# Optimization experiments

Measured on AMD Instinct MI355X. Metric: run time of the kernel, lower is better.

## Reference

```python
import jax, jax.numpy as jnp
import numpy as np
from jax import lax

WINDOW_SIZE = 11
PAD = WINDOW_SIZE // 2
L = 128.0
C1 = (0.01 * L) ** 2  # 1.6384
C2 = (0.03 * L) ** 2  # 14.7456


def _box(x, window):
    # depthwise (grouped) conv with uniform 11x11 box window, SAME padding
    return lax.conv_general_dilated(
        x, window, window_strides=(1, 1), padding=[(PAD, PAD), (PAD, PAD)],
        dimension_numbers=("NCHW", "OIHW", "NCHW"),
        feature_group_count=x.shape[1])


def setup_inputs() -> dict:
    key = jax.random.key(0)
    k1, k2 = jax.random.split(key)
    B, Ch, H, W = 64, 1, 512, 512
    img1 = jax.random.normal(k1, (B, Ch, H, W), dtype=jnp.float32)
    img2 = jax.random.normal(k2, (B, Ch, H, W), dtype=jnp.float32)
    # uniform normalized box window: outer(ones/11, ones/11) -> 1/121 each
    window = jnp.full((Ch, 1, WINDOW_SIZE, WINDOW_SIZE), 1.0 / (WINDOW_SIZE ** 2),
                      dtype=jnp.float32)
    return {"img1": img1, "img2": img2, "window": window}


def reference(img1, img2, window):
    mu1 = _box(img1, window)
    mu2 = _box(img2, window)
    mu1_sq = mu1 * mu1
    mu2_sq = mu2 * mu2
    mu1_mu2 = mu1 * mu2
    sigma1_sq = _box(img1 * img1, window) - mu1_sq
    sigma2_sq = _box(img2 * img2, window) - mu2_sq
    sigma12 = _box(img1 * img2, window) - mu1_mu2
    ret = (2.0 * mu1_mu2 + C1) / (mu1_sq + mu2_sq + C1)
    cs = (2.0 * sigma12 + C2) / (sigma1_sq + sigma2_sq + C2)
    ssim_map = ret * cs  # non_neg_flag=False, mask=None
    return 1.0 - jnp.mean(ssim_map)  # size_average=True
```

## Files before the change

kernel.cpp:

```cpp
#include <hip/hip_runtime.h>
#include <hip/hip_bf16.h>

namespace {

constexpr int IMG_H = 512;
constexpr int IMG_W = 512;
constexpr int BATCH = 64;
constexpr int RT = 16;
constexpr int WAVES = 4;
constexpr int ROWS_PER_BLOCK = RT * WAVES;
constexpr int BLOCKS_PER_IMG = IMG_H / ROWS_PER_BLOCK;
constexpr int GRID = BATCH * BLOCKS_PER_IMG;
constexpr int NPART = GRID * WAVES;
constexpr float C1 = 1.6384f;
constexpr float C2 = 14.7456f;
constexpr float INV121 = 1.0f / 121.0f;

__device__ __forceinline__ float shup1(float v) { return __shfl_up(v, 1, 64); }
__device__ __forceinline__ float shdn1(float v) { return __shfl_down(v, 1, 64); }

template <bool ADD>
__device__ __forceinline__ void hrow_acc(const float* __restrict__ p1,
                                         const float* __restrict__ p2,
                                         int r, int lane, int c0,
                                         float V[5][8])
{
  if ((unsigned)r >= (unsigned)IMG_H) return;
  const float4* a1 = reinterpret_cast<const float4*>(p1 + (size_t)r * IMG_W + c0);
  const float4* a2 = reinterpret_cast<const float4*>(p2 + (size_t)r * IMG_W + c0);
  float4 xa = a1[0], xb = a1[1];
  float4 ya = a2[0], yb = a2[1];
  float ox[8] = {xa.x, xa.y, xa.z, xa.w, xb.x, xb.y, xb.z, xb.w};
  float oy[8] = {ya.x, ya.y, ya.z, ya.w, yb.x, yb.y, yb.z, yb.w};

  float xw[18], yw[18];
#pragma unroll
  for (int i = 0; i < 8; ++i) { xw[5 + i] = ox[i]; yw[5 + i] = oy[i]; }
  const bool l0 = (lane == 0), l63 = (lane == 63);
#pragma unroll
  for (int i = 0; i < 5; ++i) {
    float tx = shup1(ox[3 + i]), ty = shup1(oy[3 + i]);
    xw[i] = l0 ? 0.f : tx;
    yw[i] = l0 ? 0.f : ty;
    float bx = shdn1(ox[i]), by = shdn1(oy[i]);
    xw[13 + i] = l63 ? 0.f : bx;
    yw[13 + i] = l63 ? 0.f : by;
  }

#pragma unroll
  for (int q = 0; q < 5; ++q) {
    float w[18];
#pragma unroll
    for (int j = 0; j < 18; ++j) {
      float xv = xw[j], yv = yw[j];
      w[j] = (q == 0) ? xv
           : (q == 1) ? yv
           : (q == 2) ? xv * xv
           : (q == 3) ? yv * yv
           : xv * yv;
    }
    float h = w[0];
#pragma unroll
    for (int j = 1; j < 11; ++j) h += w[j];
    V[q][0] += ADD ? h : -h;
#pragma unroll
    for (int k = 1; k < 8; ++k) {
      h += w[k + 10] - w[k - 1];
      V[q][k] += ADD ? h : -h;
    }
  }
}

__device__ __forceinline__ float ssim_row(const float V[5][8])
{
  float rs = 0.f;
#pragma unroll
  for (int k = 0; k < 8; ++k) {
    float mu1 = V[0][k] * INV121;
    float mu2 = V[1][k] * INV121;
    float m11 = mu1 * mu1, m22 = mu2 * mu2, m12 = mu1 * mu2;
    float s1  = V[2][k] * INV121 - m11;
    float s2  = V[3][k] * INV121 - m22;
    float s12 = V[4][k] * INV121 - m12;
    float n1 = 2.f * m12 + C1;
    float n2 = 2.f * s12 + C2;
    float d1 = m11 + m22 + C1;
    float d2 = s1 + s2 + C2;
    float den = d1 * d2;
    float rc = __builtin_amdgcn_rcpf(den);
    rc = rc * (2.f - den * rc);
    rs += (n1 * n2) * rc;
  }
  return rs;
}

}

__global__ __launch_bounds__(256, 2) void ssim_main(
    const float* __restrict__ img1, const float* __restrict__ img2,
    float* __restrict__ partials)
{
  const int tid = threadIdx.x;
  const int wave = tid >> 6;
  const int lane = tid & 63;
  const int gb = blockIdx.x;
  const int b  = gb >> 3;
  const int rb = gb & 7;
  const int y0 = rb * ROWS_PER_BLOCK + wave * RT;
  const int c0 = lane * 8;
  const float* p1 = img1 + (size_t)b * IMG_H * IMG_W;
  const float* p2 = img2 + (size_t)b * IMG_H * IMG_W;

  float V[5][8];
#pragma unroll
  for (int q = 0; q < 5; ++q)
#pragma unroll
    for (int k = 0; k < 8; ++k) V[q][k] = 0.f;

#pragma unroll 1
  for (int d = -5; d <= 5; ++d) hrow_acc<true>(p1, p2, y0 + d, lane, c0, V);

  float acc = ssim_row(V);

#pragma unroll 1
  for (int y = y0 + 1; y < y0 + RT; ++y) {
    hrow_acc<true >(p1, p2, y + 5, lane, c0, V);
    hrow_acc<false>(p1, p2, y - 6, lane, c0, V);
    acc += ssim_row(V);
  }

#pragma unroll
  for (int off = 32; off > 0; off >>= 1) acc += __shfl_down(acc, off, 64);
  if (lane == 0) partials[gb * WAVES + wave] = acc;
}

__global__ void ssim_reduce(const float* __restrict__ partials,
                            float* __restrict__ out)
{
  __shared__ double sd[256];
  const int tid = threadIdx.x;
  double s = 0.0;
  for (int i = tid; i < NPART; i += 256) s += (double)partials[i];
  sd[tid] = s;
  __syncthreads();
  for (int st = 128; st > 0; st >>= 1) {
    if (tid < st) sd[tid] += sd[tid + st];
    __syncthreads();
  }
  if (tid == 0) {
    double mean = sd[0] * (1.0 / 16777216.0);
    out[0] = (float)(1.0 - mean);
  }
}

extern "C" void kernel_launch(void* const* d_in, const int* in_sizes, int n_in,
                              void* d_out, int out_size, void* d_ws, size_t ws_size,
                              hipStream_t stream)
{
  const float* img1 = (const float*)d_in[0];
  const float* img2 = (const float*)d_in[1];
  float* out = (float*)d_out;
  float* partials = (float*)d_ws;

  ssim_main<<<dim3(GRID), dim3(256), 0, stream>>>(img1, img2, partials);
  ssim_reduce<<<dim3(1), dim3(256), 0, stream>>>(partials, out);
}
```

Measured before the change: 184.5 us.

## Swap separable box filter order: vertical running sums then horizontal pass

The kernel now keeps vertical running column sums of the five moment quantities per pixel, updated by adding the entering row and subtracting the leaving row. The horizontal 11-tap sliding sum is computed once per output row on these column sums. Before, it ran on every input row twice, once to add and once to subtract. This roughly halves the shuffle and horizontal-add work per output row. It also halves rows per wave, which doubles the grid and the halo reloads, and raises the occupancy hint to 4 blocks per CU, which may pressure registers.

```diff
diff --git a/kernel.cpp b/kernel.cpp
--- a/kernel.cpp
+++ b/kernel.cpp
@@ -6,7 +6,7 @@
 constexpr int IMG_H = 512;
 constexpr int IMG_W = 512;
 constexpr int BATCH = 64;
-constexpr int RT = 16;
+constexpr int RT = 8;
 constexpr int WAVES = 4;
 constexpr int ROWS_PER_BLOCK = RT * WAVES;
 constexpr int BLOCKS_PER_IMG = IMG_H / ROWS_PER_BLOCK;
@@ -20,10 +20,9 @@
 __device__ __forceinline__ float shdn1(float v) { return __shfl_down(v, 1, 64); }
 
 template <bool ADD>
-__device__ __forceinline__ void hrow_acc(const float* __restrict__ p1,
+__device__ __forceinline__ void vrow_acc(const float* __restrict__ p1,
                                          const float* __restrict__ p2,
-                                         int r, int lane, int c0,
-                                         float V[5][8])
+                                         int r, int c0, float V[5][8])
 {
   if ((unsigned)r >= (unsigned)IMG_H) return;
   const float4* a1 = reinterpret_cast<const float4*>(p1 + (size_t)r * IMG_W + c0);
@@ -32,56 +31,55 @@
   float4 ya = a2[0], yb = a2[1];
   float ox[8] = {xa.x, xa.y, xa.z, xa.w, xb.x, xb.y, xb.z, xb.w};
   float oy[8] = {ya.x, ya.y, ya.z, ya.w, yb.x, yb.y, yb.z, yb.w};
+#pragma unroll
+  for (int k = 0; k < 8; ++k) {
+    float x = ox[k], y = oy[k];
+    if (ADD) {
+      V[0][k] += x;       V[1][k] += y;
+      V[2][k] += x * x;   V[3][k] += y * y;   V[4][k] += x * y;
+    } else {
+      V[0][k] -= x;       V[1][k] -= y;
+      V[2][k] -= x * x;   V[3][k] -= y * y;   V[4][k] -= x * y;
+    }
+  }
+}
 
-  float xw[18], yw[18];
-#pragma unroll
-  for (int i = 0; i < 8; ++i) { xw[5 + i] = ox[i]; yw[5 + i] = oy[i]; }
+__device__ __forceinline__ float ssim_from_V(const float V[5][8], int lane)
+{
+  float H[5][8];
   const bool l0 = (lane == 0), l63 = (lane == 63);
-#pragma unroll
-  for (int i = 0; i < 5; ++i) {
-    float tx = shup1(ox[3 + i]), ty = shup1(oy[3 + i]);
-    xw[i] = l0 ? 0.f : tx;
-    yw[i] = l0 ? 0.f : ty;
-    float bx = shdn1(ox[i]), by = shdn1(oy[i]);
-    xw[13 + i] = l63 ? 0.f : bx;
-    yw[13 + i] = l63 ? 0.f : by;
-  }
-
 #pragma unroll
   for (int q = 0; q < 5; ++q) {
     float w[18];
 #pragma unroll
-    for (int j = 0; j < 18; ++j) {
-      float xv = xw[j], yv = yw[j];
-      w[j] = (q == 0) ? xv
-           : (q == 1) ? yv
-           : (q == 2) ? xv * xv
-           : (q == 3) ? yv * yv
-           : xv * yv;
+    for (int i = 0; i < 8; ++i) w[5 + i] = V[q][i];
+#pragma unroll
+    for (int i = 0; i < 5; ++i) {
+      float t = shup1(V[q][3 + i]);
+      w[i] = l0 ? 0.f : t;
+      float b = shdn1(V[q][i]);
+      w[13 + i] = l63 ? 0.f : b;
     }
     float h = w[0];
 #pragma unroll
     for (int j = 1; j < 11; ++j) h += w[j];
-    V[q][0] += ADD ? h : -h;
+    H[q][0] = h;
 #pragma unroll
     for (int k = 1; k < 8; ++k) {
       h += w[k + 10] - w[k - 1];
-      V[q][k] += ADD ? h : -h;
+      H[q][k] = h;
     }
   }
-}
 
-__device__ __forceinline__ float ssim_row(const float V[5][8])
-{
   float rs = 0.f;
 #pragma unroll
   for (int k = 0; k < 8; ++k) {
-    float mu1 = V[0][k] * INV121;
-    float mu2 = V[1][k] * INV121;
+    float mu1 = H[0][k] * INV121;
+    float mu2 = H[1][k] * INV121;
     float m11 = mu1 * mu1, m22 = mu2 * mu2, m12 = mu1 * mu2;
-    float s1  = V[2][k] * INV121 - m11;
-    float s2  = V[3][k] * INV121 - m22;
-    float s12 = V[4][k] * INV121 - m12;
+    float s1  = H[2][k] * INV121 - m11;
+    float s2  = H[3][k] * INV121 - m22;
+    float s12 = H[4][k] * INV121 - m12;
     float n1 = 2.f * m12 + C1;
     float n2 = 2.f * s12 + C2;
     float d1 = m11 + m22 + C1;
@@ -96,7 +94,7 @@
 
 }
 
-__global__ __launch_bounds__(256, 2) void ssim_main(
+__global__ __launch_bounds__(256, 4) void ssim_main(
     const float* __restrict__ img1, const float* __restrict__ img2,
     float* __restrict__ partials)
 {
@@ -104,8 +102,8 @@
   const int wave = tid >> 6;
   const int lane = tid & 63;
   const int gb = blockIdx.x;
-  const int b  = gb >> 3;
-  const int rb = gb & 7;
+  const int b  = gb >> 4;
+  const int rb = gb & 15;
   const int y0 = rb * ROWS_PER_BLOCK + wave * RT;
   const int c0 = lane * 8;
   const float* p1 = img1 + (size_t)b * IMG_H * IMG_W;
@@ -118,15 +116,15 @@
     for (int k = 0; k < 8; ++k) V[q][k] = 0.f;
 
 #pragma unroll 1
-  for (int d = -5; d <= 5; ++d) hrow_acc<true>(p1, p2, y0 + d, lane, c0, V);
+  for (int d = -5; d <= 5; ++d) vrow_acc<true>(p1, p2, y0 + d, c0, V);
 
-  float acc = ssim_row(V);
+  float acc = ssim_from_V(V, lane);
 
 #pragma unroll 1
   for (int y = y0 + 1; y < y0 + RT; ++y) {
-    hrow_acc<true >(p1, p2, y + 5, lane, c0, V);
-    hrow_acc<false>(p1, p2, y - 6, lane, c0, V);
-    acc += ssim_row(V);
+    vrow_acc<true >(p1, p2, y + 5, c0, V);
+    vrow_acc<false>(p1, p2, y - 6, c0, V);
+    acc += ssim_from_V(V, lane);
   }
 
 #pragma unroll
```

Result: slower. 194.5 us (+5.4%).
